# Performance work log

Measured on AMD Instinct MI355X. Metric: run time of the kernel, lower is better.

## Reference

```python
import jax, jax.numpy as jnp
import numpy as np

N_NODES = 50000
N_EDGES = 1600000
F_IN = 256
HID = 256
HEADS = 8
HD = HID // HEADS  # 32
SLOPE = 0.2
EPS = 1e-5


def setup_inputs() -> dict:
    key = jax.random.key(0)
    ks = jax.random.split(key, 10)
    node_features = jax.random.normal(ks[0], (N_NODES, F_IN), jnp.float32)
    edge_index = jax.random.randint(ks[1], (2, N_EDGES), 0, N_NODES, jnp.int32)
    s = 1.0 / np.sqrt(F_IN)
    W = jax.random.uniform(ks[2], (HEADS, F_IN, HD), jnp.float32, -s, s)
    bw = jax.random.uniform(ks[3], (HEADS, HD), jnp.float32, -s, s)
    sa = 1.0 / np.sqrt(2 * HD)
    A = jax.random.uniform(ks[4], (HEADS, 2 * HD), jnp.float32, -sa, sa)
    ba = jax.random.uniform(ks[5], (HEADS,), jnp.float32, -sa, sa)
    gamma = jnp.ones((HEADS, HD), jnp.float32)
    beta = jnp.zeros((HEADS, HD), jnp.float32)
    so = 1.0 / np.sqrt(HD)
    Wout = jax.random.uniform(ks[6], (HD, HID), jnp.float32, -so, so)
    bout = jax.random.uniform(ks[7], (HID,), jnp.float32, -so, so)
    return dict(node_features=node_features, edge_index=edge_index, W=W, bw=bw,
                A=A, ba=ba, gamma=gamma, beta=beta, Wout=Wout, bout=bout)


def _head(x, W, bw, a, ba, gamma, beta, tgt, src):
    h = x @ W + bw                         # [N, d]
    # attn(concat(h_i, h_j)) = h_i @ a1 + h_j @ a2 + ba  (linear over concat)
    si = h @ a[:HD]                        # [N]
    sj = h @ a[HD:]                        # [N]
    e = si[tgt] + sj[src] + ba             # [E]
    e = jnp.where(e >= 0, e, SLOPE * e)    # leaky_relu
    # scatter_softmax over edges grouped by target node (stable)
    m = jax.ops.segment_max(e, tgt, num_segments=N_NODES)
    ex = jnp.exp(e - m[tgt])
    den = jax.ops.segment_sum(ex, tgt, num_segments=N_NODES)
    alpha = ex / den[tgt]                  # [E]  (dropout in eval mode = identity)
    msg = alpha[:, None] * h[src]          # [E, d]
    agg = jax.ops.segment_sum(msg, tgt, num_segments=N_NODES)  # [N, d]
    out = agg + h                          # skip connection
    out = jnp.where(out > 0, out, jnp.expm1(out))  # ELU
    mu = out.mean(axis=-1, keepdims=True)
    var = out.var(axis=-1, keepdims=True)
    return (out - mu) * jax.lax.rsqrt(var + EPS) * gamma + beta


def reference(node_features, edge_index, W, bw, A, ba, gamma, beta, Wout, bout):
    tgt = edge_index[0]
    src = edge_index[1]
    heads = jax.vmap(_head, in_axes=(None, 0, 0, 0, 0, 0, 0, None, None))(
        node_features, W, bw, A, ba, gamma, beta, tgt, src)   # [H, N, d]
    mean = heads.mean(axis=0)                                  # [N, d]
    y = mean @ Wout + bout                                     # [N, HID]
    return jnp.where(y > 0, y, jnp.expm1(y))                   # ELU
```

## Files before the change

### kernel.cpp

```cpp
#include <hip/hip_runtime.h>
#include <hip/hip_bf16.h>
#include <hip/hip_fp16.h>

#define N_NODES 50000
#define N_EDGES 1600000
#define HEADS 8
#define HD 32
#define FIN 256
#define HID 256

typedef unsigned short u16;
typedef unsigned int u32;

typedef short s8v __attribute__((ext_vector_type(8)));
typedef float f4v __attribute__((ext_vector_type(4)));
typedef float fx4 __attribute__((ext_vector_type(4)));

__device__ __forceinline__ u32 pk2(float lo, float hi) {
  __hip_bfloat162 b = __float22bfloat162_rn(make_float2(lo, hi));
  union { __hip_bfloat162 b2; u32 u; } c;
  c.b2 = b;
  return c.u;
}

__global__ __launch_bounds__(512) void k_gemm(
    const float* __restrict__ X, const float* __restrict__ W,
    const float* __restrict__ bw, const float* __restrict__ A,
    __half* __restrict__ Hb, float* __restrict__ si, float* __restrict__ sj) {
  __shared__ __align__(16) u16 Xs[128 * 40];
  __shared__ __align__(16) u16 Wt[256 * 40];

  const int t = threadIdx.x;
  const int m0 = blockIdx.x * 128;
  const int w = t >> 6;
  const int lane = t & 63;
  const int l15 = lane & 15;
  const int quad = lane >> 4;
  const int wm = (w >> 2) * 64;
  const int wn = (w & 3) * 64;

  f4v acc[4][4];
#pragma unroll
  for (int i = 0; i < 4; i++)
#pragma unroll
    for (int j = 0; j < 4; j++) acc[i][j] = (f4v){0.f, 0.f, 0.f, 0.f};

  const int nl = t & 255;
  const int half = t >> 8;
  const int gh = nl >> 5, gd = nl & 31;

  for (int k0 = 0; k0 < FIN; k0 += 32) {
#pragma unroll
    for (int p = 0; p < 2; p++) {
      int row = p * 64 + (t >> 3);
      int f4 = t & 7;
      int node = m0 + row;
      fx4 xv = (fx4){0.f, 0.f, 0.f, 0.f};
      if (node < N_NODES)
        xv = __builtin_nontemporal_load((const fx4*)&X[node * FIN + k0 + f4 * 4]);
      u32* dst = (u32*)&Xs[row * 40 + f4 * 4];
      dst[0] = pk2(xv[0], xv[1]);
      dst[1] = pk2(xv[2], xv[3]);
    }
    {
      const float* wp = W + gh * (FIN * HD) + (k0 + half * 16) * HD + gd;
#pragma unroll
      for (int j = 0; j < 8; j++) {
        float lo = wp[(2 * j) * HD];
        float hi = wp[(2 * j + 1) * HD];
        *(u32*)&Wt[nl * 40 + half * 16 + 2 * j] = pk2(lo, hi);
      }
    }
    __syncthreads();
    s8v af[4], bf[4];
#pragma unroll
    for (int mi = 0; mi < 4; mi++)
      af[mi] = *(const s8v*)&Xs[(wm + mi * 16 + l15) * 40 + quad * 8];
#pragma unroll
    for (int ni = 0; ni < 4; ni++)
      bf[ni] = *(const s8v*)&Wt[(wn + ni * 16 + l15) * 40 + quad * 8];
#pragma unroll
    for (int mi = 0; mi < 4; mi++)
#pragma unroll
      for (int ni = 0; ni < 4; ni++)
        acc[mi][ni] = __builtin_amdgcn_mfma_f32_16x16x32_bf16(af[mi], bf[ni], acc[mi][ni], 0, 0, 0);
    __syncthreads();
  }

  const int head0 = wn >> 5;
  const int head1 = head0 + 1;
  float c1a0 = A[head0 * 64 + l15],      c1a1 = A[head0 * 64 + 16 + l15];
  float c2a0 = A[head0 * 64 + 32 + l15], c2a1 = A[head0 * 64 + 48 + l15];
  float c1b0 = A[head1 * 64 + l15],      c1b1 = A[head1 * 64 + 16 + l15];
  float c2b0 = A[head1 * 64 + 32 + l15], c2b1 = A[head1 * 64 + 48 + l15];

#pragma unroll
  for (int mi = 0; mi < 4; mi++) {
#pragma unroll
    for (int ni = 0; ni < 4; ni++) {
      float b = bw[wn + ni * 16 + l15];
#pragma unroll
      for (int r = 0; r < 4; r++) acc[mi][ni][r] += b;
    }
    const int rbase = m0 + wm + mi * 16 + quad * 4;
#pragma unroll
    for (int r = 0; r < 4; r++) {
      int node = rbase + r;
      if (node < N_NODES) {
#pragma unroll
        for (int ni = 0; ni < 4; ni++) {
          int col = wn + ni * 16 + l15;
          Hb[node * HID + col] = __float2half_rn(acc[mi][ni][r]);
        }
      }
    }
    float s1a[4], s2a[4], s1b[4], s2b[4];
#pragma unroll
    for (int r = 0; r < 4; r++) {
      s1a[r] = acc[mi][0][r] * c1a0 + acc[mi][1][r] * c1a1;
      s2a[r] = acc[mi][0][r] * c2a0 + acc[mi][1][r] * c2a1;
      s1b[r] = acc[mi][2][r] * c1b0 + acc[mi][3][r] * c1b1;
      s2b[r] = acc[mi][2][r] * c2b0 + acc[mi][3][r] * c2b1;
    }
#pragma unroll
    for (int off = 1; off <= 8; off <<= 1) {
#pragma unroll
      for (int r = 0; r < 4; r++) {
        s1a[r] += __shfl_xor(s1a[r], off);
        s2a[r] += __shfl_xor(s2a[r], off);
        s1b[r] += __shfl_xor(s1b[r], off);
        s2b[r] += __shfl_xor(s2b[r], off);
      }
    }
    if (l15 == 0) {
#pragma unroll
      for (int r = 0; r < 4; r++) {
        int node = rbase + r;
        if (node < N_NODES) {
          si[node * HEADS + head0] = s1a[r];
          sj[node * HEADS + head0] = s2a[r];
          si[node * HEADS + head1] = s1b[r];
          sj[node * HEADS + head1] = s2b[r];
        }
      }
    }
  }
}

__global__ void k_hist(const int* __restrict__ tgt, int* __restrict__ cnt) {
  int e = blockIdx.x * 256 + threadIdx.x;
  if (e < N_EDGES) atomicAdd(&cnt[tgt[e]], 1);
}

__global__ __launch_bounds__(256) void k_scan1(const int* __restrict__ cnt,
    int* __restrict__ excl, int* __restrict__ bsum) {
  __shared__ int s[256];
  const int t = threadIdx.x;
  const int i = blockIdx.x * 256 + t;
  int v = (i < N_NODES) ? cnt[i] : 0;
  s[t] = v;
  __syncthreads();
  int x = v;
  for (int off = 1; off < 256; off <<= 1) {
    int y = (t >= off) ? s[t - off] : 0;
    __syncthreads();
    x += y;
    s[t] = x;
    __syncthreads();
  }
  if (i < N_NODES) excl[i] = x - v;
  if (t == 255) bsum[blockIdx.x] = x;
}

__global__ __launch_bounds__(256) void k_scan2(const int* __restrict__ bsum,
                                               int* __restrict__ boff) {
  __shared__ int s[256];
  const int t = threadIdx.x;
  int v = (t < 196) ? bsum[t] : 0;
  s[t] = v;
  __syncthreads();
  int x = v;
  for (int off = 1; off < 256; off <<= 1) {
    int y = (t >= off) ? s[t - off] : 0;
    __syncthreads();
    x += y;
    s[t] = x;
    __syncthreads();
  }
  if (t < 196) boff[t] = x - v;
}

__global__ void k_scan3(const int* __restrict__ excl, const int* __restrict__ boff,
                        int* __restrict__ rowptr, int* __restrict__ cursor) {
  int i = blockIdx.x * 256 + threadIdx.x;
  if (i < N_NODES) {
    int v = excl[i] + boff[blockIdx.x];
    rowptr[i] = v;
    cursor[i] = v;
  }
}

__global__ void k_scatter(const int* __restrict__ tgt, const int* __restrict__ src,
                          int* __restrict__ cursor, int* __restrict__ sortedSrc) {
  int e = blockIdx.x * 256 + threadIdx.x;
  if (e < N_EDGES) {
    int tg = tgt[e];
    int pos = atomicAdd(&cursor[tg], 1);
    sortedSrc[pos] = src[e];
  }
}

__global__ __launch_bounds__(256) void k_fused(
    const __half* __restrict__ Hb, const float* __restrict__ si,
    const float* __restrict__ sj, const float* __restrict__ ba,
    const float* __restrict__ gamma, const float* __restrict__ beta,
    const float* __restrict__ Wout, const float* __restrict__ bout,
    const int* __restrict__ rowptr, const int* __restrict__ cnt,
    const int* __restrict__ sortedSrc, float* __restrict__ out) {
  const int t = threadIdx.x;
  const int lane = t & 63;
  const int n = blockIdx.x * 4 + (t >> 6);
  const int cg = lane & 31;
  const int es = lane >> 5;
  const int hh = cg >> 2;
  const int start = rowptr[n];
  const int deg = cnt[n];

  const float sb = si[n * HEADS + hh] + ba[hh];
  const char* hbBase = (const char*)Hb + 16 * cg;
  const int* ss = sortedSrc + start;

  float acc[8] = {0.f, 0.f, 0.f, 0.f, 0.f, 0.f, 0.f, 0.f};
  float den = 0.f;
#pragma unroll 4
  for (int slot = es; slot < deg; slot += 2) {
    int s = __builtin_nontemporal_load(ss + slot);
    float e = sb + sj[s * HEADS + hh];
    e = (e >= 0.f) ? e : 0.2f * e;
    float exv = __expf(e);
    float4 hb4 = *(const float4*)(hbBase + (size_t)s * (HID * 2));
    const __half2* hp = (const __half2*)&hb4;
#pragma unroll
    for (int d = 0; d < 4; d++) {
      acc[2 * d]     += exv * __low2float(hp[d]);
      acc[2 * d + 1] += exv * __high2float(hp[d]);
    }
    den += exv;
  }
#pragma unroll
  for (int j = 0; j < 8; j++) acc[j] += __shfl_xor(acc[j], 32);
  den += __shfl_xor(den, 32);

  float4 h4 = *(const float4*)((const char*)Hb + (size_t)n * (HID * 2) + 16 * cg);
  const __half2* hq = (const __half2*)&h4;
  float inv = (deg > 0) ? __fdividef(1.f, den) : 0.f;
  float v[8], sum = 0.f, sq = 0.f;
#pragma unroll
  for (int j = 0; j < 8; j++) {
    float hv = (j & 1) ? __high2float(hq[j >> 1]) : __low2float(hq[j >> 1]);
    float x = acc[j] * inv + hv;
    x = (x > 0.f) ? x : (__expf(x) - 1.f);
    v[j] = x;
    sum += x;
    sq += x * x;
  }
  sum += __shfl_xor(sum, 1); sq += __shfl_xor(sq, 1);
  sum += __shfl_xor(sum, 2); sq += __shfl_xor(sq, 2);
  float mu = sum * (1.f / 32.f);
  float var = sq * (1.f / 32.f) - mu * mu;
  float rstd = rsqrtf(var + 1e-5f);
  fx4 g0 = *(const fx4*)&gamma[cg * 8];
  fx4 g1 = *(const fx4*)&gamma[cg * 8 + 4];
  fx4 b0 = *(const fx4*)&beta[cg * 8];
  fx4 b1 = *(const fx4*)&beta[cg * 8 + 4];
  float m2[8];
#pragma unroll
  for (int j = 0; j < 8; j++) {
    float g = (j < 4) ? g0[j] : g1[j - 4];
    float bb = (j < 4) ? b0[j] : b1[j - 4];
    m2[j] = (v[j] - mu) * rstd * g + bb;
  }
#pragma unroll
  for (int j = 0; j < 8; j++) {
    m2[j] += __shfl_xor(m2[j], 4);
    m2[j] += __shfl_xor(m2[j], 8);
    m2[j] += __shfl_xor(m2[j], 16);
  }

  fx4 y = *(const fx4*)&bout[4 * lane];
#pragma unroll
  for (int q = 0; q < 4; q++) {
    float mv[8];
#pragma unroll
    for (int j = 0; j < 8; j++) mv[j] = __shfl(m2[j], q) * 0.125f;
#pragma unroll
    for (int j = 0; j < 8; j++) {
      fx4 w4 = *(const fx4*)&Wout[(q * 8 + j) * HID + 4 * lane];
      y += mv[j] * w4;
    }
  }
#pragma unroll
  for (int c = 0; c < 4; c++) y[c] = (y[c] > 0.f) ? y[c] : (__expf(y[c]) - 1.f);
  __builtin_nontemporal_store(y, (fx4*)&out[(size_t)n * HID + 4 * lane]);
}

extern "C" void kernel_launch(void* const* d_in, const int* in_sizes, int n_in,
                              void* d_out, int out_size, void* d_ws, size_t ws_size,
                              hipStream_t stream) {
  const float* X     = (const float*)d_in[0];
  const int*   EI    = (const int*)d_in[1];
  const float* W     = (const float*)d_in[2];
  const float* bw    = (const float*)d_in[3];
  const float* A     = (const float*)d_in[4];
  const float* ba    = (const float*)d_in[5];
  const float* gamma = (const float*)d_in[6];
  const float* beta  = (const float*)d_in[7];
  const float* Wout  = (const float*)d_in[8];
  const float* bout  = (const float*)d_in[9];
  float* out = (float*)d_out;
  const int* tgt = EI;
  const int* src = EI + N_EDGES;

  char* ws = (char*)d_ws;
  size_t off = 0;
  auto alloc = [&](size_t bytes) -> void* {
    void* p = ws + off;
    off += bytes;
    off = (off + 255) & ~(size_t)255;
    return p;
  };
  __half* Hb       = (__half*)alloc((size_t)N_NODES * HID * 2);
  float* si        = (float*)alloc((size_t)N_NODES * HEADS * 4);
  float* sj        = (float*)alloc((size_t)N_NODES * HEADS * 4);
  int*   cnt       = (int*)  alloc((size_t)N_NODES * 4);
  int*   excl      = (int*)  alloc((size_t)N_NODES * 4);
  int*   bsum      = (int*)  alloc(256 * 4);
  int*   boff      = (int*)  alloc(256 * 4);
  int*   rowptr    = (int*)  alloc((size_t)N_NODES * 4);
  int*   cursor    = (int*)  alloc((size_t)N_NODES * 4);
  int*   sortedSrc = (int*)  alloc((size_t)N_EDGES * 4);

  hipMemsetAsync(cnt, 0, (size_t)N_NODES * 4, stream);
  k_hist<<<(N_EDGES + 255) / 256, 256, 0, stream>>>(tgt, cnt);
  k_scan1<<<196, 256, 0, stream>>>(cnt, excl, bsum);
  k_scan2<<<1, 256, 0, stream>>>(bsum, boff);
  k_scan3<<<196, 256, 0, stream>>>(excl, boff, rowptr, cursor);
  k_scatter<<<(N_EDGES + 255) / 256, 256, 0, stream>>>(tgt, src, cursor, sortedSrc);
  k_gemm<<<(N_NODES + 127) / 128, 512, 0, stream>>>(X, W, bw, A, Hb, si, sj);
  k_fused<<<(N_NODES + 3) / 4, 256, 0, stream>>>(Hb, si, sj, ba, gamma, beta,
                                                 Wout, bout, rowptr, cnt,
                                                 sortedSrc, out);
}
```

Measured before the change: 495.9 us.

## Prepack W to bf16, use rank-based CSR scatter, and order nodes by degree

Three independent changes. A new kernel converts W to a bf16, column-major buffer once, so the GEMM loads 16-byte vectors instead of doing strided fp32 loads and repacking on every k-tile. The histogram now records each edge's rank, which lets the scatter write directly without a second atomic pass over a cursor array. A degree-bucket counting sort builds a node permutation so the fused aggregation kernel processes high-degree nodes first, aiming at better load balance; the cost is several extra small launches and an extra edge-sized rank buffer.

```diff
diff --git a/kernel.cpp b/kernel.cpp
--- a/kernel.cpp
+++ b/kernel.cpp
@@ -23,8 +23,17 @@
   return c.u;
 }
 
+__global__ __launch_bounds__(256) void k_prepw(const float* __restrict__ W,
+                                               u16* __restrict__ Wp) {
+  int id = blockIdx.x * 256 + threadIdx.x;
+  int col = id >> 8;
+  int k = id & 255;
+  int h = col >> 5, d = col & 31;
+  Wp[col * 256 + k] = (u16)(pk2(W[h * 8192 + k * 32 + d], 0.f) & 0xFFFFu);
+}
+
 __global__ __launch_bounds__(512) void k_gemm(
-    const float* __restrict__ X, const float* __restrict__ W,
+    const float* __restrict__ X, const u16* __restrict__ Wp,
     const float* __restrict__ bw, const float* __restrict__ A,
     __half* __restrict__ Hb, float* __restrict__ si, float* __restrict__ sj) {
   __shared__ __align__(16) u16 Xs[128 * 40];
@@ -45,9 +54,8 @@
 #pragma unroll
     for (int j = 0; j < 4; j++) acc[i][j] = (f4v){0.f, 0.f, 0.f, 0.f};
 
-  const int nl = t & 255;
-  const int half = t >> 8;
-  const int gh = nl >> 5, gd = nl & 31;
+  const int wcol = t >> 2;
+  const int wpart = t & 3;
 
   for (int k0 = 0; k0 < FIN; k0 += 32) {
 #pragma unroll
@@ -62,14 +70,11 @@
       dst[0] = pk2(xv[0], xv[1]);
       dst[1] = pk2(xv[2], xv[3]);
     }
-    {
-      const float* wp = W + gh * (FIN * HD) + (k0 + half * 16) * HD + gd;
-#pragma unroll
-      for (int j = 0; j < 8; j++) {
-        float lo = wp[(2 * j) * HD];
-        float hi = wp[(2 * j + 1) * HD];
-        *(u32*)&Wt[nl * 40 + half * 16 + 2 * j] = pk2(lo, hi);
-      }
+#pragma unroll
+    for (int c2 = 0; c2 < 2; c2++) {
+      int cc = wcol + c2 * 128;
+      *(fx4*)&Wt[cc * 40 + wpart * 8] =
+          *(const fx4*)&Wp[cc * 256 + k0 + wpart * 8];
     }
     __syncthreads();
     s8v af[4], bf[4];
@@ -147,9 +152,10 @@
   }
 }
 
-__global__ void k_hist(const int* __restrict__ tgt, int* __restrict__ cnt) {
+__global__ void k_hist(const int* __restrict__ tgt, int* __restrict__ cnt,
+                       int* __restrict__ rank) {
   int e = blockIdx.x * 256 + threadIdx.x;
-  if (e < N_EDGES) atomicAdd(&cnt[tgt[e]], 1);
+  if (e < N_EDGES) rank[e] = atomicAdd(&cnt[tgt[e]], 1);
 }
 
 __global__ __launch_bounds__(256) void k_scan1(const int* __restrict__ cnt,
@@ -191,22 +197,47 @@
 }
 
 __global__ void k_scan3(const int* __restrict__ excl, const int* __restrict__ boff,
-                        int* __restrict__ rowptr, int* __restrict__ cursor) {
+                        int* __restrict__ rowptr) {
   int i = blockIdx.x * 256 + threadIdx.x;
-  if (i < N_NODES) {
-    int v = excl[i] + boff[blockIdx.x];
-    rowptr[i] = v;
-    cursor[i] = v;
-  }
+  if (i < N_NODES) rowptr[i] = excl[i] + boff[blockIdx.x];
 }
 
 __global__ void k_scatter(const int* __restrict__ tgt, const int* __restrict__ src,
-                          int* __restrict__ cursor, int* __restrict__ sortedSrc) {
+                          const int* __restrict__ rowptr, const int* __restrict__ rank,
+                          int* __restrict__ sortedSrc) {
   int e = blockIdx.x * 256 + threadIdx.x;
-  if (e < N_EDGES) {
-    int tg = tgt[e];
-    int pos = atomicAdd(&cursor[tg], 1);
-    sortedSrc[pos] = src[e];
+  if (e < N_EDGES) sortedSrc[rowptr[tgt[e]] + rank[e]] = src[e];
+}
+
+__global__ void k_dhist(const int* __restrict__ cnt, int* __restrict__ dcnt) {
+  int n = blockIdx.x * 256 + threadIdx.x;
+  if (n < N_NODES) atomicAdd(&dcnt[255 - min(cnt[n], 255)], 1);
+}
+
+__global__ __launch_bounds__(256) void k_dscan(const int* __restrict__ dcnt,
+                                               int* __restrict__ dcur) {
+  __shared__ int s[256];
+  const int t = threadIdx.x;
+  int v = dcnt[t];
+  s[t] = v;
+  __syncthreads();
+  int x = v;
+  for (int off = 1; off < 256; off <<= 1) {
+    int y = (t >= off) ? s[t - off] : 0;
+    __syncthreads();
+    x += y;
+    s[t] = x;
+    __syncthreads();
+  }
+  dcur[t] = x - v;
+}
+
+__global__ void k_dscatter(const int* __restrict__ cnt, int* __restrict__ dcur,
+                           int* __restrict__ perm) {
+  int n = blockIdx.x * 256 + threadIdx.x;
+  if (n < N_NODES) {
+    int pos = atomicAdd(&dcur[255 - min(cnt[n], 255)], 1);
+    perm[pos] = n;
   }
 }
 
@@ -216,10 +247,11 @@
     const float* __restrict__ gamma, const float* __restrict__ beta,
     const float* __restrict__ Wout, const float* __restrict__ bout,
     const int* __restrict__ rowptr, const int* __restrict__ cnt,
-    const int* __restrict__ sortedSrc, float* __restrict__ out) {
+    const int* __restrict__ sortedSrc, const int* __restrict__ perm,
+    float* __restrict__ out) {
   const int t = threadIdx.x;
   const int lane = t & 63;
-  const int n = blockIdx.x * 4 + (t >> 6);
+  const int n = perm[blockIdx.x * 4 + (t >> 6)];
   const int cg = lane & 31;
   const int es = lane >> 5;
   const int hh = cg >> 2;
@@ -286,7 +318,6 @@
     m2[j] += __shfl_xor(m2[j], 8);
     m2[j] += __shfl_xor(m2[j], 16);
   }
-
   fx4 y = *(const fx4*)&bout[4 * lane];
 #pragma unroll
   for (int q = 0; q < 4; q++) {
@@ -337,17 +368,26 @@
   int*   bsum      = (int*)  alloc(256 * 4);
   int*   boff      = (int*)  alloc(256 * 4);
   int*   rowptr    = (int*)  alloc((size_t)N_NODES * 4);
-  int*   cursor    = (int*)  alloc((size_t)N_NODES * 4);
+  int*   rank      = (int*)  alloc((size_t)N_EDGES * 4);
   int*   sortedSrc = (int*)  alloc((size_t)N_EDGES * 4);
+  int*   dcnt      = (int*)  alloc(256 * 4);
+  int*   dcur      = (int*)  alloc(256 * 4);
+  int*   perm      = (int*)  alloc((size_t)N_NODES * 4);
+  u16*   Wp        = (u16*)  alloc((size_t)HID * FIN * 2);
 
   hipMemsetAsync(cnt, 0, (size_t)N_NODES * 4, stream);
-  k_hist<<<(N_EDGES + 255) / 256, 256, 0, stream>>>(tgt, cnt);
+  hipMemsetAsync(dcnt, 0, 256 * 4, stream);
+  k_prepw<<<256, 256, 0, stream>>>(W, Wp);
+  k_hist<<<(N_EDGES + 255) / 256, 256, 0, stream>>>(tgt, cnt, rank);
   k_scan1<<<196, 256, 0, stream>>>(cnt, excl, bsum);
   k_scan2<<<1, 256, 0, stream>>>(bsum, boff);
-  k_scan3<<<196, 256, 0, stream>>>(excl, boff, rowptr, cursor);
-  k_scatter<<<(N_EDGES + 255) / 256, 256, 0, stream>>>(tgt, src, cursor, sortedSrc);
-  k_gemm<<<(N_NODES + 127) / 128, 512, 0, stream>>>(X, W, bw, A, Hb, si, sj);
+  k_scan3<<<196, 256, 0, stream>>>(excl, boff, rowptr);
+  k_scatter<<<(N_EDGES + 255) / 256, 256, 0, stream>>>(tgt, src, rowptr, rank, sortedSrc);
+  k_dhist<<<196, 256, 0, stream>>>(cnt, dcnt);
+  k_dscan<<<1, 256, 0, stream>>>(dcnt, dcur);
+  k_dscatter<<<196, 256, 0, stream>>>(cnt, dcur, perm);
+  k_gemm<<<(N_NODES + 127) / 128, 512, 0, stream>>>(X, Wp, bw, A, Hb, si, sj);
   k_fused<<<(N_NODES + 3) / 4, 256, 0, stream>>>(Hb, si, sj, ba, gamma, beta,
                                                  Wout, bout, rowptr, cnt,
-                                                 sortedSrc, out);
-}
+                                                 sortedSrc, perm, out);
+}
```

New measurement: 588.6 us. 1.19x slower.
